# Performance work log

Hardware: AMD Instinct MI355X
Metric: run time of the kernel (lower is better)

Reference implementation:

```python
import jax, jax.numpy as jnp
import numpy as np

N_NODES = 50000
N_EDGES = 600000
EPS = 1e-5


def setup_inputs() -> dict:
    key = jax.random.key(0)
    ks = jax.random.split(key, 8)
    return {
        "x": jax.random.normal(ks[0], (N_NODES, 128), dtype=jnp.float32),
        "src": jax.random.randint(ks[1], (N_EDGES,), 0, N_NODES, dtype=jnp.int32),
        "dst": jax.random.randint(ks[2], (N_EDGES,), 0, N_NODES, dtype=jnp.int32),
        "weight": jax.random.uniform(ks[3], (N_EDGES,), dtype=jnp.float32),
        "W1": jax.random.normal(ks[4], (128, 128), dtype=jnp.float32) * 0.05,
        "b1": jnp.zeros((128,), dtype=jnp.float32),
        "gamma1": jnp.ones((128,), dtype=jnp.float32),
        "beta1": jnp.zeros((128,), dtype=jnp.float32),
        "W2": jax.random.normal(ks[5], (128, 64), dtype=jnp.float32) * 0.05,
        "b2": jnp.zeros((64,), dtype=jnp.float32),
        "gamma2": jnp.ones((64,), dtype=jnp.float32),
        "beta2": jnp.zeros((64,), dtype=jnp.float32),
        "W3": jax.random.normal(ks[6], (64, 32), dtype=jnp.float32) * 0.05,
        "b3": jnp.zeros((32,), dtype=jnp.float32),
    }


def _batchnorm(h, gamma, beta):
    # BatchNorm1d in training mode over the node axis (biased variance)
    mean = jnp.mean(h, axis=0)
    var = jnp.mean((h - mean) ** 2, axis=0)
    return gamma * (h - mean) * jax.lax.rsqrt(var + EPS) + beta


def reference(x, src, dst, weight, W1, b1, gamma1, beta1, W2, b2, gamma2, beta2, W3, b3):
    n = x.shape[0]
    # GCNConv: add self-loops with weight 1, symmetric normalization
    loop = jnp.arange(n, dtype=src.dtype)
    src_f = jnp.concatenate([src, loop])  # [E+N]
    dst_f = jnp.concatenate([dst, loop])
    w_f = jnp.concatenate([weight, jnp.ones((n,), dtype=weight.dtype)])
    deg = jax.ops.segment_sum(w_f, dst_f, num_segments=n)  # [N]
    dinv = jnp.where(deg > 0, deg ** -0.5, 0.0)
    norm = dinv[src_f] * w_f * dinv[dst_f]  # [E+N], same for every layer

    def conv(h, W, b):
        h = h @ W  # [N, out]
        msg = norm[:, None] * h[src_f]  # gather + edge scale
        return jax.ops.segment_sum(msg, dst_f, num_segments=n) + b

    h = conv(x, W1, b1)
    h = jax.nn.relu(_batchnorm(h, gamma1, beta1))
    h = conv(h, W2, b2)
    h = jax.nn.relu(_batchnorm(h, gamma2, beta2))
    h = conv(h, W3, b3)  # final BatchNorm is dropped by net[:-1] in encode()
    return h
```

## Files before the change

### kernel.cpp

```cpp
#include <hip/hip_runtime.h>
#include <hip/hip_bf16.h>

#define NN 50000
#define NE 600000
#define SLOTS 48

typedef unsigned short ushortT;
typedef __attribute__((ext_vector_type(8))) short bf16x8;
typedef __attribute__((ext_vector_type(4))) float f32x4;

__device__ __forceinline__ ushortT f2bfbits(float f) {
    __hip_bfloat16 h = __float2bfloat16(f);
    return *reinterpret_cast<ushortT*>(&h);
}

__device__ __forceinline__ float4 unpack_bf4(uint2 p) {
    float4 r;
    r.x = __uint_as_float(p.x << 16);
    r.y = __uint_as_float(p.x & 0xffff0000u);
    r.z = __uint_as_float(p.y << 16);
    r.w = __uint_as_float(p.y & 0xffff0000u);
    return r;
}

template <int K, int M>
__device__ __forceinline__ void pack_w_dev(const float* __restrict__ W,
                                           ushortT* __restrict__ Wp, int t) {
    constexpr int KC = K / 32;
    constexpr int CT = M / 16;
    if (t >= CT * KC * 64) return;
    int l = t & 63;
    int q = (t >> 6) % KC;
    int c = t / (64 * KC);
    int m = l & 15, quad = l >> 4;
    alignas(16) ushortT tmp[8];
#pragma unroll
    for (int j = 0; j < 8; ++j)
        tmp[j] = f2bfbits(W[(size_t)(q * 32 + quad * 8 + j) * M + c * 16 + m]);
    *reinterpret_cast<uint4*>(&Wp[(size_t)t * 8]) = *reinterpret_cast<const uint4*>(tmp);
}

__global__ void __launch_bounds__(256) prep_kernel(const float* __restrict__ W1,
                                                   const float* __restrict__ W2,
                                                   const float* __restrict__ W3,
                                                   ushortT* __restrict__ Wp1,
                                                   ushortT* __restrict__ Wp2,
                                                   ushortT* __restrict__ Wp3,
                                                   int* __restrict__ counts,
                                                   float* __restrict__ sums, int n) {
    int b = blockIdx.x, tid = threadIdx.x;
    if (b < 8) {
        pack_w_dev<128, 128>(W1, Wp1, b * 256 + tid);
    } else if (b < 12) {
        pack_w_dev<128, 64>(W2, Wp2, (b - 8) * 256 + tid);
    } else if (b < 13) {
        pack_w_dev<64, 32>(W3, Wp3, (b - 12) * 256 + tid);
    } else {
        int i = (b - 13) * 256 + tid;
        if (i < n) counts[i] = 0;
        if (b == 13) sums[tid] = 0.f;
    }
}

template <typename AT, int K, int M, bool FUSEBN>
__device__ __forceinline__ void gemm_dev(int bid, const AT* __restrict__ A,
                                         const ushortT* __restrict__ Wp,
                                         const float* __restrict__ sums,
                                         const float* __restrict__ gamma,
                                         const float* __restrict__ beta,
                                         ushortT* __restrict__ out, int N) {
    constexpr int KC = K / 32;
    constexpr int CT = M / 16;
    int wave = threadIdx.x >> 6;
    int lane = threadIdx.x & 63;
    int m = lane & 15, quad = lane >> 4;
    int rowbase = bid * 64 + wave * 16;
    int arow = min(rowbase + m, N - 1);

    f32x4 acc[CT] = {};
    const float invN = 1.0f / (float)N;

#pragma unroll
    for (int q = 0; q < KC; ++q) {
        int kb = q * 32 + quad * 8;
        float av[8];
        if constexpr (sizeof(AT) == 4) {
            const float* ap = (const float*)A + (size_t)arow * K + kb;
            float4 lo = *reinterpret_cast<const float4*>(ap);
            float4 hi = *reinterpret_cast<const float4*>(ap + 4);
            av[0] = lo.x; av[1] = lo.y; av[2] = lo.z; av[3] = lo.w;
            av[4] = hi.x; av[5] = hi.y; av[6] = hi.z; av[7] = hi.w;
        } else {
            const ushortT* ap = (const ushortT*)A + (size_t)arow * K + kb;
            uint4 p = *reinterpret_cast<const uint4*>(ap);
            float4 lo = unpack_bf4(make_uint2(p.x, p.y));
            float4 hi = unpack_bf4(make_uint2(p.z, p.w));
            av[0] = lo.x; av[1] = lo.y; av[2] = lo.z; av[3] = lo.w;
            av[4] = hi.x; av[5] = hi.y; av[6] = hi.z; av[7] = hi.w;
        }
        if constexpr (FUSEBN) {
#pragma unroll
            for (int j = 0; j < 8; ++j) {
                int k = kb + j;
                float mean = sums[k] * invN;
                float var = fmaf(-mean, mean, sums[K + k] * invN);
                var = var > 0.f ? var : 0.f;
                float sc = gamma[k] * rsqrtf(var + 1e-5f);
                float sh = fmaf(-mean, sc, beta[k]);
                av[j] = fmaxf(fmaf(av[j], sc, sh), 0.f);
            }
        }
        bf16x8 af;
#pragma unroll
        for (int j = 0; j < 8; ++j) af[j] = (short)f2bfbits(av[j]);
#pragma unroll
        for (int c = 0; c < CT; ++c) {
            bf16x8 bf = *reinterpret_cast<const bf16x8*>(
                &Wp[(((size_t)c * KC + q) * 64 + lane) * 8]);
            acc[c] = __builtin_amdgcn_mfma_f32_16x16x32_bf16(af, bf, acc[c], 0, 0, 0);
        }
    }
#pragma unroll
    for (int c = 0; c < CT; ++c) {
#pragma unroll
        for (int r = 0; r < 4; ++r) {
            int row = rowbase + quad * 4 + r;
            if (row < N) out[(size_t)row * M + c * 16 + m] = f2bfbits(acc[c][r]);
        }
    }
}

__global__ void __launch_bounds__(256) fill_gemm1_kernel(
    const int* __restrict__ src, const int* __restrict__ dst, const float* __restrict__ w,
    int* __restrict__ counts, int2* __restrict__ col_sw, int E,
    const float* __restrict__ x, const ushortT* __restrict__ Wp1,
    ushortT* __restrict__ hlin, int N, int FB) {
    if ((int)blockIdx.x < FB) {
        int e = blockIdx.x * 256 + threadIdx.x;
        if (e < E) {
            int d = dst[e];
            int pos = atomicAdd(&counts[d], 1);
            if (pos < SLOTS) col_sw[(size_t)pos * N + d] = make_int2(src[e], __float_as_int(w[e]));
        }
        return;
    }
    gemm_dev<float, 128, 128, false>(blockIdx.x - FB, x, Wp1, nullptr, nullptr, nullptr, hlin, N);
}

template <typename AT, int K, int M, bool FUSEBN>
__global__ void __launch_bounds__(256) mfma_gemm(const AT* __restrict__ A,
                                                 const ushortT* __restrict__ Wp,
                                                 const float* __restrict__ sums,
                                                 const float* __restrict__ gamma,
                                                 const float* __restrict__ beta,
                                                 ushortT* __restrict__ out, int N) {
    gemm_dev<AT, K, M, FUSEBN>(blockIdx.x, A, Wp, sums, gamma, beta, out, N);
}

__global__ void deg_dinv_kernel(const int* __restrict__ counts, const int2* __restrict__ col_sw,
                                float* __restrict__ dinv, int n) {
    int i = blockIdx.x * blockDim.x + threadIdx.x;
    if (i >= n) return;
    int c = min(counts[i], SLOTS);
    float s = 1.0f;
    for (int j = 0; j < c; ++j) s += __int_as_float(col_sw[(size_t)j * n + i].y);
    dinv[i] = rsqrtf(s);
}

__global__ void norm_bucket_kernel(const int* __restrict__ counts, int2* __restrict__ col_sw,
                                   const float* __restrict__ dinv, int n) {
    int idx = blockIdx.x * blockDim.x + threadIdx.x;
    if (idx >= n * SLOTS) return;
    int j = idx / n;
    int node = idx - j * n;
    if (j >= min(counts[node], SLOTS)) return;
    int2 sw = col_sw[idx];
    col_sw[idx].y = __float_as_int(dinv[sw.x] * __int_as_float(sw.y) * dinv[node]);
}

template <int C, bool OUTBF, bool ZERO>
__global__ void __launch_bounds__(256) csr_agg_kernel(const ushortT* __restrict__ hbf,
                                                      const int* __restrict__ counts,
                                                      const int2* __restrict__ col_sw,
                                                      const float* __restrict__ dinv,
                                                      const float* __restrict__ bias,
                                                      void* __restrict__ out,
                                                      float* __restrict__ sums, int N) {
    if (ZERO && blockIdx.x == 0) sums[threadIdx.x] = 0.f;
    constexpr int C8 = C / 8;
    int idx = blockIdx.x * 256 + threadIdx.x;
    if (idx >= N * C8) return;
    int node = idx / C8;
    int c8 = idx - node * C8;
    const uint4* h8 = reinterpret_cast<const uint4*>(hbf);
    int cnt = min(counts[node], SLOTS);
    float di = dinv[node];
    float sl = di * di;
    uint4 hp = h8[idx];
    float4 hlo = unpack_bf4(make_uint2(hp.x, hp.y));
    float4 hhi = unpack_bf4(make_uint2(hp.z, hp.w));
    float4 blo = *reinterpret_cast<const float4*>(&bias[8 * c8]);
    float4 bhi = *reinterpret_cast<const float4*>(&bias[8 * c8 + 4]);
    float4 alo, ahi;
    alo.x = fmaf(sl, hlo.x, blo.x); alo.y = fmaf(sl, hlo.y, blo.y);
    alo.z = fmaf(sl, hlo.z, blo.z); alo.w = fmaf(sl, hlo.w, blo.w);
    ahi.x = fmaf(sl, hhi.x, bhi.x); ahi.y = fmaf(sl, hhi.y, bhi.y);
    ahi.z = fmaf(sl, hhi.z, bhi.z); ahi.w = fmaf(sl, hhi.w, bhi.w);
    const int2* cs = col_sw + node;
    int j = 0;
    for (; j + 2 <= cnt; j += 2) {
        int2 sw0 = cs[(size_t)j * N];
        int2 sw1 = cs[(size_t)(j + 1) * N];
        uint4 p0 = h8[(size_t)sw0.x * C8 + c8];
        uint4 p1 = h8[(size_t)sw1.x * C8 + c8];
        float n0 = __int_as_float(sw0.y);
        float n1 = __int_as_float(sw1.y);
        float4 l0 = unpack_bf4(make_uint2(p0.x, p0.y));
        float4 h0 = unpack_bf4(make_uint2(p0.z, p0.w));
        float4 l1 = unpack_bf4(make_uint2(p1.x, p1.y));
        float4 h1 = unpack_bf4(make_uint2(p1.z, p1.w));
        alo.x = fmaf(n0, l0.x, alo.x); alo.y = fmaf(n0, l0.y, alo.y);
        alo.z = fmaf(n0, l0.z, alo.z); alo.w = fmaf(n0, l0.w, alo.w);
        ahi.x = fmaf(n0, h0.x, ahi.x); ahi.y = fmaf(n0, h0.y, ahi.y);
        ahi.z = fmaf(n0, h0.z, ahi.z); ahi.w = fmaf(n0, h0.w, ahi.w);
        alo.x = fmaf(n1, l1.x, alo.x); alo.y = fmaf(n1, l1.y, alo.y);
        alo.z = fmaf(n1, l1.z, alo.z); alo.w = fmaf(n1, l1.w, alo.w);
        ahi.x = fmaf(n1, h1.x, ahi.x); ahi.y = fmaf(n1, h1.y, ahi.y);
        ahi.z = fmaf(n1, h1.z, ahi.z); ahi.w = fmaf(n1, h1.w, ahi.w);
    }
    if (j < cnt) {
        int2 sw = cs[(size_t)j * N];
        float nrm = __int_as_float(sw.y);
        uint4 p = h8[(size_t)sw.x * C8 + c8];
        float4 lo = unpack_bf4(make_uint2(p.x, p.y));
        float4 hi = unpack_bf4(make_uint2(p.z, p.w));
        alo.x = fmaf(nrm, lo.x, alo.x); alo.y = fmaf(nrm, lo.y, alo.y);
        alo.z = fmaf(nrm, lo.z, alo.z); alo.w = fmaf(nrm, lo.w, alo.w);
        ahi.x = fmaf(nrm, hi.x, ahi.x); ahi.y = fmaf(nrm, hi.y, ahi.y);
        ahi.z = fmaf(nrm, hi.z, ahi.z); ahi.w = fmaf(nrm, hi.w, ahi.w);
    }
    if constexpr (OUTBF) {
        alignas(16) ushortT tmp[8];
        tmp[0] = f2bfbits(alo.x); tmp[1] = f2bfbits(alo.y);
        tmp[2] = f2bfbits(alo.z); tmp[3] = f2bfbits(alo.w);
        tmp[4] = f2bfbits(ahi.x); tmp[5] = f2bfbits(ahi.y);
        tmp[6] = f2bfbits(ahi.z); tmp[7] = f2bfbits(ahi.w);
        reinterpret_cast<uint4*>(out)[idx] = *reinterpret_cast<const uint4*>(tmp);
    } else {
        float4* o4 = reinterpret_cast<float4*>(out);
        o4[idx * 2] = alo;
        o4[idx * 2 + 1] = ahi;
    }
}

#define BN_GRID 104
template <int C>
__global__ void __launch_bounds__(256) bn_stats_kernel(const ushortT* __restrict__ hbf,
                                                       float* __restrict__ sums, int N) {
    constexpr int C4 = C / 4;
    constexpr int SPB = 256 / C4;
    __shared__ float4 sm1[256], sm2[256];
    int tid = threadIdx.x;
    int c4 = tid % C4;
    int r0 = blockIdx.x * SPB + tid / C4;
    int stride = gridDim.x * SPB;
    const uint2* h2 = reinterpret_cast<const uint2*>(hbf);
    float4 s = make_float4(0.f, 0.f, 0.f, 0.f);
    float4 s2 = make_float4(0.f, 0.f, 0.f, 0.f);
    for (int r = r0; r < N; r += stride) {
        float4 v = unpack_bf4(h2[(size_t)r * C4 + c4]);
        s.x += v.x; s.y += v.y; s.z += v.z; s.w += v.w;
        s2.x = fmaf(v.x, v.x, s2.x);
        s2.y = fmaf(v.y, v.y, s2.y);
        s2.z = fmaf(v.z, v.z, s2.z);
        s2.w = fmaf(v.w, v.w, s2.w);
    }
    sm1[tid] = s; sm2[tid] = s2;
    __syncthreads();
#pragma unroll
    for (int off = 128; off >= C4; off >>= 1) {
        if (tid < off) {
            float4 a = sm1[tid + off], b = sm2[tid + off];
            float4 u = sm1[tid], v = sm2[tid];
            u.x += a.x; u.y += a.y; u.z += a.z; u.w += a.w;
            v.x += b.x; v.y += b.y; v.z += b.z; v.w += b.w;
            sm1[tid] = u; sm2[tid] = v;
        }
        __syncthreads();
    }
    if (tid < C4) {
        float4 a = sm1[tid], b = sm2[tid];
        unsafeAtomicAdd(&sums[4 * tid + 0], a.x);
        unsafeAtomicAdd(&sums[4 * tid + 1], a.y);
        unsafeAtomicAdd(&sums[4 * tid + 2], a.z);
        unsafeAtomicAdd(&sums[4 * tid + 3], a.w);
        unsafeAtomicAdd(&sums[C + 4 * tid + 0], b.x);
        unsafeAtomicAdd(&sums[C + 4 * tid + 1], b.y);
        unsafeAtomicAdd(&sums[C + 4 * tid + 2], b.z);
        unsafeAtomicAdd(&sums[C + 4 * tid + 3], b.w);
    }
}

extern "C" void kernel_launch(void* const* d_in, const int* in_sizes, int n_in,
                              void* d_out, int out_size, void* d_ws, size_t ws_size,
                              hipStream_t stream) {
    const float* x      = (const float*)d_in[0];
    const int*   src    = (const int*)d_in[1];
    const int*   dst    = (const int*)d_in[2];
    const float* weight = (const float*)d_in[3];
    const float* W1     = (const float*)d_in[4];
    const float* b1     = (const float*)d_in[5];
    const float* gamma1 = (const float*)d_in[6];
    const float* beta1  = (const float*)d_in[7];
    const float* W2     = (const float*)d_in[8];
    const float* b2     = (const float*)d_in[9];
    const float* gamma2 = (const float*)d_in[10];
    const float* beta2  = (const float*)d_in[11];
    const float* W3     = (const float*)d_in[12];
    const float* b3     = (const float*)d_in[13];
    float* out = (float*)d_out;

    const int N = NN, E = NE;

    char* ws = (char*)d_ws;
    size_t off = 0;
    auto alloc = [&](size_t bytes) {
        size_t r = off;
        off += (bytes + 255) & ~(size_t)255;
        return r;
    };
    float*   dinv    = (float*)(ws + alloc((size_t)N * 4));
    int*     counts  = (int*)(ws + alloc((size_t)N * 4));
    int2*    col_sw  = (int2*)(ws + alloc((size_t)N * SLOTS * 8));
    ushortT* hlin_bf = (ushortT*)(ws + alloc((size_t)N * 128 * 2));
    ushortT* hagg_bf = (ushortT*)(ws + alloc((size_t)N * 128 * 2));
    ushortT* Wp1     = (ushortT*)(ws + alloc(128 * 128 * 2));
    ushortT* Wp2     = (ushortT*)(ws + alloc(128 * 64 * 2));
    ushortT* Wp3     = (ushortT*)(ws + alloc(64 * 32 * 2));
    float*   sums    = (float*)(ws + alloc(256 * 4));

    dim3 blk(256);
    auto grd = [](long long n) { return dim3((unsigned)((n + 255) / 256)); };
    const int GB = (N + 63) / 64;
    const int DB = (N + 255) / 256;
    const int FB = (E + 255) / 256;

    prep_kernel<<<13 + DB, blk, 0, stream>>>(W1, W2, W3, Wp1, Wp2, Wp3, counts, sums, N);

    ushortT* h1agg = hagg_bf;
    fill_gemm1_kernel<<<FB + GB, blk, 0, stream>>>(src, dst, weight, counts, col_sw, E,
                                                   x, Wp1, hlin_bf, N, FB);
    deg_dinv_kernel<<<DB, blk, 0, stream>>>(counts, col_sw, dinv, N);
    norm_bucket_kernel<<<grd((long long)N * SLOTS), blk, 0, stream>>>(counts, col_sw, dinv, N);

    csr_agg_kernel<128, true, false><<<grd((long long)N * 16), blk, 0, stream>>>(
        hlin_bf, counts, col_sw, dinv, b1, h1agg, sums, N);
    bn_stats_kernel<128><<<BN_GRID, 256, 0, stream>>>(h1agg, sums, N);

    ushortT* h2agg = hagg_bf;
    mfma_gemm<ushortT, 128, 64, true><<<GB, blk, 0, stream>>>(
        h1agg, Wp2, sums, gamma1, beta1, hlin_bf, N);
    csr_agg_kernel<64, true, true><<<grd((long long)N * 8), blk, 0, stream>>>(
        hlin_bf, counts, col_sw, dinv, b2, h2agg, sums, N);
    bn_stats_kernel<64><<<BN_GRID, 256, 0, stream>>>(h2agg, sums, N);

    mfma_gemm<ushortT, 64, 32, true><<<GB, blk, 0, stream>>>(
        h2agg, Wp3, sums, gamma2, beta2, hlin_bf, N);
    csr_agg_kernel<32, false, false><<<grd((long long)N * 4), blk, 0, stream>>>(
        hlin_bf, counts, col_sw, dinv, b3, out, sums, N);
}
```

Baseline: 271.9 us.

## Compute edge norm on the fly in aggregation, drop norm pass, unfuse fill/gemm

Removes the norm_bucket_kernel pass that rewrote every bucket slot with the normalized weight. The aggregation kernels now compute dinv[src]*w*dinv[dst] inline, with an extra dinv gather per edge in each of the three layers. The fused fill+GEMM1 kernel is split back into separate bucket-fill and GEMM launches, and the gather loop is unrolled from 2 to 4 edges for more memory-level parallelism.

```diff
diff --git a/kernel.cpp b/kernel.cpp
--- a/kernel.cpp
+++ b/kernel.cpp
@@ -62,19 +62,40 @@
     }
 }
 
+__global__ void bucket_fill_kernel(const int* __restrict__ src, const int* __restrict__ dst,
+                                   const float* __restrict__ w, int* __restrict__ counts,
+                                   int2* __restrict__ col_sw, int E, int n) {
+    int e = blockIdx.x * 256 + threadIdx.x;
+    if (e < E) {
+        int d = dst[e];
+        int pos = atomicAdd(&counts[d], 1);
+        if (pos < SLOTS) col_sw[(size_t)pos * n + d] = make_int2(src[e], __float_as_int(w[e]));
+    }
+}
+
+__global__ void deg_dinv_kernel(const int* __restrict__ counts, const int2* __restrict__ col_sw,
+                                float* __restrict__ dinv, int n) {
+    int i = blockIdx.x * 256 + threadIdx.x;
+    if (i >= n) return;
+    int c = min(counts[i], SLOTS);
+    float s = 1.0f;
+    for (int j = 0; j < c; ++j) s += __int_as_float(col_sw[(size_t)j * n + i].y);
+    dinv[i] = rsqrtf(s);
+}
+
 template <typename AT, int K, int M, bool FUSEBN>
-__device__ __forceinline__ void gemm_dev(int bid, const AT* __restrict__ A,
-                                         const ushortT* __restrict__ Wp,
-                                         const float* __restrict__ sums,
-                                         const float* __restrict__ gamma,
-                                         const float* __restrict__ beta,
-                                         ushortT* __restrict__ out, int N) {
+__global__ void __launch_bounds__(256) mfma_gemm(const AT* __restrict__ A,
+                                                 const ushortT* __restrict__ Wp,
+                                                 const float* __restrict__ sums,
+                                                 const float* __restrict__ gamma,
+                                                 const float* __restrict__ beta,
+                                                 ushortT* __restrict__ out, int N) {
     constexpr int KC = K / 32;
     constexpr int CT = M / 16;
     int wave = threadIdx.x >> 6;
     int lane = threadIdx.x & 63;
     int m = lane & 15, quad = lane >> 4;
-    int rowbase = bid * 64 + wave * 16;
+    int rowbase = blockIdx.x * 64 + wave * 16;
     int arow = min(rowbase + m, N - 1);
 
     f32x4 acc[CT] = {};
@@ -128,54 +149,6 @@
             if (row < N) out[(size_t)row * M + c * 16 + m] = f2bfbits(acc[c][r]);
         }
     }
-}
-
-__global__ void __launch_bounds__(256) fill_gemm1_kernel(
-    const int* __restrict__ src, const int* __restrict__ dst, const float* __restrict__ w,
-    int* __restrict__ counts, int2* __restrict__ col_sw, int E,
-    const float* __restrict__ x, const ushortT* __restrict__ Wp1,
-    ushortT* __restrict__ hlin, int N, int FB) {
-    if ((int)blockIdx.x < FB) {
-        int e = blockIdx.x * 256 + threadIdx.x;
-        if (e < E) {
-            int d = dst[e];
-            int pos = atomicAdd(&counts[d], 1);
-            if (pos < SLOTS) col_sw[(size_t)pos * N + d] = make_int2(src[e], __float_as_int(w[e]));
-        }
-        return;
-    }
-    gemm_dev<float, 128, 128, false>(blockIdx.x - FB, x, Wp1, nullptr, nullptr, nullptr, hlin, N);
-}
-
-template <typename AT, int K, int M, bool FUSEBN>
-__global__ void __launch_bounds__(256) mfma_gemm(const AT* __restrict__ A,
-                                                 const ushortT* __restrict__ Wp,
-                                                 const float* __restrict__ sums,
-                                                 const float* __restrict__ gamma,
-                                                 const float* __restrict__ beta,
-                                                 ushortT* __restrict__ out, int N) {
-    gemm_dev<AT, K, M, FUSEBN>(blockIdx.x, A, Wp, sums, gamma, beta, out, N);
-}
-
-__global__ void deg_dinv_kernel(const int* __restrict__ counts, const int2* __restrict__ col_sw,
-                                float* __restrict__ dinv, int n) {
-    int i = blockIdx.x * blockDim.x + threadIdx.x;
-    if (i >= n) return;
-    int c = min(counts[i], SLOTS);
-    float s = 1.0f;
-    for (int j = 0; j < c; ++j) s += __int_as_float(col_sw[(size_t)j * n + i].y);
-    dinv[i] = rsqrtf(s);
-}
-
-__global__ void norm_bucket_kernel(const int* __restrict__ counts, int2* __restrict__ col_sw,
-                                   const float* __restrict__ dinv, int n) {
-    int idx = blockIdx.x * blockDim.x + threadIdx.x;
-    if (idx >= n * SLOTS) return;
-    int j = idx / n;
-    int node = idx - j * n;
-    if (j >= min(counts[node], SLOTS)) return;
-    int2 sw = col_sw[idx];
-    col_sw[idx].y = __float_as_int(dinv[sw.x] * __int_as_float(sw.y) * dinv[node]);
 }
 
 template <int C, bool OUTBF, bool ZERO>
@@ -207,38 +180,38 @@
     ahi.x = fmaf(sl, hhi.x, bhi.x); ahi.y = fmaf(sl, hhi.y, bhi.y);
     ahi.z = fmaf(sl, hhi.z, bhi.z); ahi.w = fmaf(sl, hhi.w, bhi.w);
     const int2* cs = col_sw + node;
+
+#define ACC_EDGE(SW, DV)                                            \
+    {                                                               \
+        float nrm = DV * __int_as_float((SW).y) * di;               \
+        uint4 p = h8[(size_t)(SW).x * C8 + c8];                     \
+        float4 lo = unpack_bf4(make_uint2(p.x, p.y));               \
+        float4 hi = unpack_bf4(make_uint2(p.z, p.w));               \
+        alo.x = fmaf(nrm, lo.x, alo.x); alo.y = fmaf(nrm, lo.y, alo.y); \
+        alo.z = fmaf(nrm, lo.z, alo.z); alo.w = fmaf(nrm, lo.w, alo.w); \
+        ahi.x = fmaf(nrm, hi.x, ahi.x); ahi.y = fmaf(nrm, hi.y, ahi.y); \
+        ahi.z = fmaf(nrm, hi.z, ahi.z); ahi.w = fmaf(nrm, hi.w, ahi.w); \
+    }
+
     int j = 0;
-    for (; j + 2 <= cnt; j += 2) {
-        int2 sw0 = cs[(size_t)j * N];
+    for (; j + 4 <= cnt; j += 4) {
+        int2 sw0 = cs[(size_t)(j + 0) * N];
         int2 sw1 = cs[(size_t)(j + 1) * N];
-        uint4 p0 = h8[(size_t)sw0.x * C8 + c8];
-        uint4 p1 = h8[(size_t)sw1.x * C8 + c8];
-        float n0 = __int_as_float(sw0.y);
-        float n1 = __int_as_float(sw1.y);
-        float4 l0 = unpack_bf4(make_uint2(p0.x, p0.y));
-        float4 h0 = unpack_bf4(make_uint2(p0.z, p0.w));
-        float4 l1 = unpack_bf4(make_uint2(p1.x, p1.y));
-        float4 h1 = unpack_bf4(make_uint2(p1.z, p1.w));
-        alo.x = fmaf(n0, l0.x, alo.x); alo.y = fmaf(n0, l0.y, alo.y);
-        alo.z = fmaf(n0, l0.z, alo.z); alo.w = fmaf(n0, l0.w, alo.w);
-        ahi.x = fmaf(n0, h0.x, ahi.x); ahi.y = fmaf(n0, h0.y, ahi.y);
-        ahi.z = fmaf(n0, h0.z, ahi.z); ahi.w = fmaf(n0, h0.w, ahi.w);
-        alo.x = fmaf(n1, l1.x, alo.x); alo.y = fmaf(n1, l1.y, alo.y);
-        alo.z = fmaf(n1, l1.z, alo.z); alo.w = fmaf(n1, l1.w, alo.w);
-        ahi.x = fmaf(n1, h1.x, ahi.x); ahi.y = fmaf(n1, h1.y, ahi.y);
-        ahi.z = fmaf(n1, h1.z, ahi.z); ahi.w = fmaf(n1, h1.w, ahi.w);
-    }
-    if (j < cnt) {
+        int2 sw2 = cs[(size_t)(j + 2) * N];
+        int2 sw3 = cs[(size_t)(j + 3) * N];
+        float d0 = dinv[sw0.x], d1 = dinv[sw1.x], d2 = dinv[sw2.x], d3 = dinv[sw3.x];
+        ACC_EDGE(sw0, d0);
+        ACC_EDGE(sw1, d1);
+        ACC_EDGE(sw2, d2);
+        ACC_EDGE(sw3, d3);
+    }
+    for (; j < cnt; ++j) {
         int2 sw = cs[(size_t)j * N];
-        float nrm = __int_as_float(sw.y);
-        uint4 p = h8[(size_t)sw.x * C8 + c8];
-        float4 lo = unpack_bf4(make_uint2(p.x, p.y));
-        float4 hi = unpack_bf4(make_uint2(p.z, p.w));
-        alo.x = fmaf(nrm, lo.x, alo.x); alo.y = fmaf(nrm, lo.y, alo.y);
-        alo.z = fmaf(nrm, lo.z, alo.z); alo.w = fmaf(nrm, lo.w, alo.w);
-        ahi.x = fmaf(nrm, hi.x, ahi.x); ahi.y = fmaf(nrm, hi.y, ahi.y);
-        ahi.z = fmaf(nrm, hi.z, ahi.z); ahi.w = fmaf(nrm, hi.w, ahi.w);
-    }
+        float dv = dinv[sw.x];
+        ACC_EDGE(sw, dv);
+    }
+#undef ACC_EDGE
+
     if constexpr (OUTBF) {
         alignas(16) ushortT tmp[8];
         tmp[0] = f2bfbits(alo.x); tmp[1] = f2bfbits(alo.y);
@@ -343,16 +316,14 @@
     auto grd = [](long long n) { return dim3((unsigned)((n + 255) / 256)); };
     const int GB = (N + 63) / 64;
     const int DB = (N + 255) / 256;
-    const int FB = (E + 255) / 256;
 
     prep_kernel<<<13 + DB, blk, 0, stream>>>(W1, W2, W3, Wp1, Wp2, Wp3, counts, sums, N);
+    bucket_fill_kernel<<<grd(E), blk, 0, stream>>>(src, dst, weight, counts, col_sw, E, N);
+    mfma_gemm<float, 128, 128, false><<<GB, blk, 0, stream>>>(
+        x, Wp1, nullptr, nullptr, nullptr, hlin_bf, N);
+    deg_dinv_kernel<<<DB, blk, 0, stream>>>(counts, col_sw, dinv, N);
 
     ushortT* h1agg = hagg_bf;
-    fill_gemm1_kernel<<<FB + GB, blk, 0, stream>>>(src, dst, weight, counts, col_sw, E,
-                                                   x, Wp1, hlin_bf, N, FB);
-    deg_dinv_kernel<<<DB, blk, 0, stream>>>(counts, col_sw, dinv, N);
-    norm_bucket_kernel<<<grd((long long)N * SLOTS), blk, 0, stream>>>(counts, col_sw, dinv, N);
-
     csr_agg_kernel<128, true, false><<<grd((long long)N * 16), blk, 0, stream>>>(
         hlin_bf, counts, col_sw, dinv, b1, h1agg, sums, N);
     bn_stats_kernel<128><<<BN_GRID, 256, 0, stream>>>(h1agg, sums, N);
```

New measurement: 266.4 us. 1.02x faster.
